# Performance work log

Measured on AMD Instinct MI355X. Metric: run time of the kernel, lower is better.

Reference implementation:

```python
import jax, jax.numpy as jnp
import numpy as np

TEMPERATURE = 0.07
BASE_TEMPERATURE = 0.07
EPS = 1e-10


def setup_inputs() -> dict:
    key = jax.random.key(0)
    k1, k2, k3 = jax.random.split(key, 3)
    bsz, n_views, d = 4096, 2, 256
    features = jax.random.normal(k1, (bsz, n_views, d), dtype=jnp.float32)
    # L2-normalize views as is standard for SupCon inputs (keeps logits sane)
    features = features / jnp.linalg.norm(features, axis=-1, keepdims=True)
    va_labels = jax.random.normal(k2, (bsz, 2), dtype=jnp.float32)
    batch_belong_diaID = jax.random.randint(k3, (bsz,), 0, 512, dtype=jnp.int64)
    return {
        "features": features,
        "va_labels": va_labels,
        "batch_belong_diaID": batch_belong_diaID,
        "thres_dict": 1,
    }


def reference(features, va_labels, batch_belong_diaID, thres_dict):
    bsz, n_views, d = features.shape
    dtype = features.dtype

    # --- vectorized mask construction (replaces O(bsz^2) python loops) ---
    eye = jnp.eye(bsz, dtype=bool)
    same_dia = batch_belong_diaID[:, None] == batch_belong_diaID[None, :]
    diff = va_labels[:, None, :] - va_labels[None, :, :]          # [bsz, bsz, 2]
    euclid = jnp.sqrt(jnp.sum(diff * diff, axis=-1))              # [bsz, bsz]
    close_va = euclid < thres_dict
    # final mask: diagonal | same dialogue | VA-close (off-diag terms; diag already 1)
    mask = (eye | same_dia | close_va).astype(dtype)
    mask = jax.lax.stop_gradient(mask)  # mask build is non-differentiable in torch too

    # --- contrastive loss (contrast_mode='one') ---
    # torch.cat(torch.unbind(features, 1), 0): view-major stacking
    contrast_feature = features.transpose(1, 0, 2).reshape(n_views * bsz, d)
    anchor_feature = features[:, 0]                               # anchor_count = 1

    logits = jnp.matmul(anchor_feature, contrast_feature.T) / TEMPERATURE  # [bsz, n_views*bsz]
    logits = logits - jax.lax.stop_gradient(jnp.max(logits, axis=1, keepdims=True))

    mask_t = jnp.tile(mask, (1, n_views))                          # [bsz, n_views*bsz]
    # logits_mask: zero out self-contrast (column i for anchor row i)
    idx = jnp.arange(bsz)
    logits_mask = jnp.ones((bsz, n_views * bsz), dtype=dtype).at[idx, idx].set(0.0)
    mask_t = mask_t * logits_mask

    exp_logits = jnp.exp(logits) * logits_mask
    log_prob = logits - jnp.log(jnp.sum(exp_logits, axis=1, keepdims=True) + EPS)

    mean_log_prob_pos = jnp.sum(mask_t * log_prob, axis=1) / (jnp.sum(mask_t, axis=1) + EPS)
    loss = jnp.mean(-mean_log_prob_pos)  # anchor_count=1 -> plain mean over bsz
    return loss
```

## Files before the change

kernel.cpp:

```cpp
#include <hip/hip_runtime.h>
#include <hip/hip_bf16.h>

#define BSZ   4096
#define NCON  8192
#define DFEAT 256
#define C2    20.60992914f
#define LN2   0.6931471806f

#define BJM 32
#define BI 128
#define NJT 8
#define JSTRIP_M (NJT * BJM)

typedef __attribute__((ext_vector_type(8))) short short8;
typedef __attribute__((ext_vector_type(4))) float f32x4;

__device__ __forceinline__ unsigned short f2bf(float f) {
    __hip_bfloat16 h = __float2bfloat16(f);
    return *reinterpret_cast<unsigned short*>(&h);
}

__device__ __forceinline__ void gload_lds16(const void* g, void* l) {
    __builtin_amdgcn_global_load_lds(
        (const __attribute__((address_space(1))) unsigned int*)g,
        (__attribute__((address_space(3))) unsigned int*)l,
        16, 0, 0);
}

__device__ __forceinline__ void gload_reg16(const void* p, short8& dst) {
    unsigned long long a = (unsigned long long)p;
    asm volatile("global_load_dwordx4 %0, %1, off"
                 : "=v"(dst) : "v"(a));
}


__global__ __launch_bounds__(256) void k_prep(const float* __restrict__ feat,
                                              unsigned short* __restrict__ con,
                                              float* __restrict__ acc) {
    int idx = blockIdx.x * 256 + threadIdx.x;
    int e = idx * 4;
    int j = e >> 8;
    int k = e & 255;
    int src = (j < BSZ) ? ((j * 2) * DFEAT + k)
                        : (((j - BSZ) * 2 + 1) * DFEAT + k);
    float4 f = *(const float4*)(feat + src);
    ushort4 o;
    o.x = f2bf(f.x); o.y = f2bf(f.y); o.z = f2bf(f.z); o.w = f2bf(f.w);
    *(ushort4*)(con + e) = o;
    if (idx < 3 * BSZ) acc[idx] = 0.0f;
}

__global__ __launch_bounds__(256, 2) void k_main(const __hip_bfloat16* __restrict__ conp,
                                                 const float* __restrict__ va,
                                                 const int* __restrict__ dia,
                                                 const int* __restrict__ thr_ptr,
                                                 float* __restrict__ Srow,
                                                 float* __restrict__ Arow,
                                                 float* __restrict__ Brow) {
    __shared__ short lX[2][2][BJM * DFEAT];
    __shared__ float s_vjx[JSTRIP_M], s_vjy[JSTRIP_M];
    __shared__ int   s_dj[JSTRIP_M];

    const int tid  = threadIdx.x;
    const int lane = tid & 63;
    const int wv   = tid >> 6;
    const int l15  = lane & 15;
    const int hi   = lane >> 4;
    const int jmbase = blockIdx.x * JSTRIP_M;
    const int ibase  = blockIdx.y * BI + wv * 32;
    const short* cs = (const short*)conp;

    auto stageX = [&](int buf, int jt) {
        #pragma unroll
        for (int v = 0; v < 2; ++v) {
            #pragma unroll
            for (int q = 0; q < 4; ++q) {
                int e   = q * 2048 + tid * 8;
                int col = e & 63;
                int row = (e >> 6) & 31;
                int k2  = e >> 11;
                int scol = col ^ ((row & 7) << 3);
                gload_lds16(cs + (size_t)(jmbase + jt * BJM + row + v * BSZ) * DFEAT
                               + k2 * 64 + scol,
                            &lX[buf][v][e]);
            }
        }
    };

    stageX(0, 0);

    const short* yrow0 = cs + (size_t)(ibase + l15) * DFEAT + hi * 8;
    short8 y[2][8];
    #pragma unroll
    for (int n = 0; n < 2; ++n)
        #pragma unroll
        for (int s = 0; s < 8; ++s)
            gload_reg16(yrow0 + (size_t)n * 16 * DFEAT + s * 32, y[n][s]);

    if (tid < JSTRIP_M) {
        int jm = jmbase + tid;
        s_vjx[tid] = va[2 * jm]; s_vjy[tid] = va[2 * jm + 1]; s_dj[tid] = dia[jm];
    }

    int raw = *thr_ptr;
    float t_ = (raw > 0 && raw < 100000) ? (float)raw : __int_as_float(raw);
    float thres2 = t_ * t_;

    float vix[2], viy[2]; int di[2], ig[2];
    #pragma unroll
    for (int n = 0; n < 2; ++n) {
        ig[n] = ibase + n * 16 + l15;
        vix[n] = va[2 * ig[n]]; viy[n] = va[2 * ig[n] + 1]; di[n] = dia[ig[n]];
    }

    float sp[2] = {0.f, 0.f};
    float ap[2] = {0.f, 0.f};
    float bp[2] = {0.f, 0.f};

    __syncthreads();
    asm volatile("s_waitcnt vmcnt(0)" ::: "memory");
    __builtin_amdgcn_sched_barrier(0);

    for (int jt = 0; jt < NJT; ++jt) {
        const int cur = jt & 1;
        if (jt < NJT - 1) stageX(cur ^ 1, jt + 1);

        f32x4 acc[2][2][2];
        #pragma unroll
        for (int v = 0; v < 2; ++v)
            #pragma unroll
            for (int m = 0; m < 2; ++m)
                #pragma unroll
                for (int n = 0; n < 2; ++n)
                    acc[v][m][n] = (f32x4){0.f, 0.f, 0.f, 0.f};

        __builtin_amdgcn_s_setprio(1);
        #pragma unroll
        for (int s = 0; s < 8; ++s) {
            const int base = (s >> 1) * 4096;
            const int colb = (s & 1) * 64 + hi * 16;
            short8 xf[2][2];
            #pragma unroll
            for (int v = 0; v < 2; ++v)
                #pragma unroll
                for (int m = 0; m < 2; ++m) {
                    int row = m * 16 + l15;
                    xf[v][m] = *(const short8*)((const char*)&lX[cur][v][0]
                                 + base + row * 128 + (colb ^ ((row & 7) << 4)));
                }
            #pragma unroll
            for (int v = 0; v < 2; ++v)
                #pragma unroll
                for (int m = 0; m < 2; ++m)
                    #pragma unroll
                    for (int n = 0; n < 2; ++n)
                        acc[v][m][n] = __builtin_amdgcn_mfma_f32_16x16x32_bf16(
                            xf[v][m], y[n][s], acc[v][m][n], 0, 0, 0);
        }
        __builtin_amdgcn_s_setprio(0);

        const int jt0 = jt * BJM;
        #pragma unroll
        for (int m = 0; m < 2; ++m)
            #pragma unroll
            for (int r = 0; r < 4; ++r) {
                const int jl  = jt0 + m * 16 + hi * 4 + r;
                const int jmg = jmbase + jl;
                float vjx = s_vjx[jl], vjy = s_vjy[jl];
                int dj = s_dj[jl];
                #pragma unroll
                for (int n = 0; n < 2; ++n) {
                    float l0 = __builtin_fmaf(acc[0][m][n][r], C2, -C2);
                    float l1 = __builtin_fmaf(acc[1][m][n][r], C2, -C2);
                    float dx = vix[n] - vjx, dy = viy[n] - vjy;
                    bool diag = (ig[n] == jmg);
                    bool mk = (di[n] == dj) | (dx * dx + dy * dy < thres2);
                    float e0 = diag ? 0.0f : exp2f(l0);
                    float e1 = exp2f(l1);
                    sp[n] += e0 + e1;
                    float mm = mk ? 1.0f : 0.0f;
                    ap[n] = __builtin_fmaf(mm, l0 + l1, ap[n]);
                    bp[n] += mm;
                }
            }
        __syncthreads();
    }

    #pragma unroll
    for (int n = 0; n < 2; ++n) {
        float s = sp[n], a = ap[n], b = bp[n];
        s += __shfl_xor(s, 16, 64);  a += __shfl_xor(a, 16, 64);  b += __shfl_xor(b, 16, 64);
        s += __shfl_xor(s, 32, 64);  a += __shfl_xor(a, 32, 64);  b += __shfl_xor(b, 32, 64);
        if (hi == 0) {
            atomicAdd(&Srow[ig[n]], s);
            atomicAdd(&Arow[ig[n]], a * LN2);
            atomicAdd(&Brow[ig[n]], b);
        }
    }
}

__global__ __launch_bounds__(256) void k_final(const float* __restrict__ S,
                                               const float* __restrict__ A,
                                               const float* __restrict__ B,
                                               float* __restrict__ out) {
    __shared__ float red[256];
    float sum = 0.f;
    for (int i = threadIdx.x; i < BSZ; i += 256) {
        float b = 2.0f * B[i] - 1.0f;
        float v = (A[i] - b * logf(S[i] + 1e-10f)) / (b + 1e-10f);
        sum += -v;
    }
    red[threadIdx.x] = sum;
    __syncthreads();
    for (int s = 128; s > 0; s >>= 1) {
        if (threadIdx.x < s) red[threadIdx.x] += red[threadIdx.x + s];
        __syncthreads();
    }
    if (threadIdx.x == 0) out[0] = red[0] / (float)BSZ;
}

extern "C" void kernel_launch(void* const* d_in, const int* in_sizes, int n_in,
                              void* d_out, int out_size, void* d_ws, size_t ws_size,
                              hipStream_t stream) {
    const float* feat = (const float*)d_in[0];
    const float* va   = (const float*)d_in[1];
    const int*   dia  = (const int*)d_in[2];
    const int*   thr  = (const int*)d_in[3];

    unsigned short* con = (unsigned short*)d_ws;
    float* acc = (float*)((char*)d_ws + (size_t)NCON * DFEAT * 2);
    float* out = (float*)d_out;

    k_prep<<<(NCON * DFEAT / 4 + 255) / 256, 256, 0, stream>>>(feat, con, acc);

    dim3 grid(BSZ / JSTRIP_M, BSZ / BI);
    k_main<<<grid, 256, 0, stream>>>((const __hip_bfloat16*)con, va, dia, thr,
                                     acc, acc + BSZ, acc + 2 * BSZ);

    k_final<<<1, 256, 0, stream>>>(acc, acc + BSZ, acc + 2 * BSZ, out);
}
```

Baseline: 47.01 us.

## Use 512-thread blocks with a four-stage LDS pipeline and per-view mask accounting

Doubles the anchor rows per block by going to 512 threads, so each staged contrast tile is reused by twice as many waves. Replaces double buffering with a 4-deep LDS ring that keeps three tiles in flight, using explicit vmcnt waits and a single s_barrier per tile in place of two __syncthreads. Also computes the positive mask and counts separately for the two views, so the self column is excluded only for view 0, and the final kernel uses the count directly instead of 2B-1. The larger LDS footprint and single-block occupancy can reduce latency hiding, and the hand-set vmcnt values must match the number of loads issued per thread.

```diff
diff --git a/kernel.cpp b/kernel.cpp
--- a/kernel.cpp
+++ b/kernel.cpp
@@ -8,7 +8,7 @@
 #define LN2   0.6931471806f
 
 #define BJM 32
-#define BI 128
+#define BI 256
 #define NJT 8
 #define JSTRIP_M (NJT * BJM)
 
@@ -50,14 +50,14 @@
     if (idx < 3 * BSZ) acc[idx] = 0.0f;
 }
 
-__global__ __launch_bounds__(256, 2) void k_main(const __hip_bfloat16* __restrict__ conp,
+__global__ __launch_bounds__(512, 1) void k_main(const __hip_bfloat16* __restrict__ conp,
                                                  const float* __restrict__ va,
                                                  const int* __restrict__ dia,
                                                  const int* __restrict__ thr_ptr,
                                                  float* __restrict__ Srow,
                                                  float* __restrict__ Arow,
                                                  float* __restrict__ Brow) {
-    __shared__ short lX[2][2][BJM * DFEAT];
+    __shared__ short lX[4][2][BJM * DFEAT];
     __shared__ float s_vjx[JSTRIP_M], s_vjy[JSTRIP_M];
     __shared__ int   s_dj[JSTRIP_M];
 
@@ -74,8 +74,8 @@
         #pragma unroll
         for (int v = 0; v < 2; ++v) {
             #pragma unroll
-            for (int q = 0; q < 4; ++q) {
-                int e   = q * 2048 + tid * 8;
+            for (int q = 0; q < 2; ++q) {
+                int e   = q * 4096 + tid * 8;
                 int col = e & 63;
                 int row = (e >> 6) & 31;
                 int k2  = e >> 11;
@@ -88,7 +88,7 @@
     };
 
     stageX(0, 0);
-
+    __builtin_amdgcn_sched_barrier(0);
     const short* yrow0 = cs + (size_t)(ibase + l15) * DFEAT + hi * 8;
     short8 y[2][8];
     #pragma unroll
@@ -96,6 +96,11 @@
         #pragma unroll
         for (int s = 0; s < 8; ++s)
             gload_reg16(yrow0 + (size_t)n * 16 * DFEAT + s * 32, y[n][s]);
+    __builtin_amdgcn_sched_barrier(0);
+    stageX(1, 1);
+    __builtin_amdgcn_sched_barrier(0);
+    stageX(2, 2);
+    __builtin_amdgcn_sched_barrier(0);
 
     if (tid < JSTRIP_M) {
         int jm = jmbase + tid;
@@ -117,14 +122,15 @@
     float ap[2] = {0.f, 0.f};
     float bp[2] = {0.f, 0.f};
 
-    __syncthreads();
-    asm volatile("s_waitcnt vmcnt(0)" ::: "memory");
-    __builtin_amdgcn_sched_barrier(0);
-
-    for (int jt = 0; jt < NJT; ++jt) {
-        const int cur = jt & 1;
-        if (jt < NJT - 1) stageX(cur ^ 1, jt + 1);
-
+    #pragma unroll
+    for (int t = 0; t < NJT; ++t) {
+        if (t <= 5)      asm volatile("s_waitcnt vmcnt(8)" ::: "memory");
+        else if (t == 6) asm volatile("s_waitcnt vmcnt(4)" ::: "memory");
+        else             asm volatile("s_waitcnt vmcnt(0)" ::: "memory");
+        __builtin_amdgcn_sched_barrier(0);
+        __builtin_amdgcn_s_barrier();
+
+        const int cur = t & 3;
         f32x4 acc[2][2][2];
         #pragma unroll
         for (int v = 0; v < 2; ++v)
@@ -134,7 +140,6 @@
                 for (int n = 0; n < 2; ++n)
                     acc[v][m][n] = (f32x4){0.f, 0.f, 0.f, 0.f};
 
-        __builtin_amdgcn_s_setprio(1);
         #pragma unroll
         for (int s = 0; s < 8; ++s) {
             const int base = (s >> 1) * 4096;
@@ -157,9 +162,8 @@
                         acc[v][m][n] = __builtin_amdgcn_mfma_f32_16x16x32_bf16(
                             xf[v][m], y[n][s], acc[v][m][n], 0, 0, 0);
         }
-        __builtin_amdgcn_s_setprio(0);
-
-        const int jt0 = jt * BJM;
+
+        const int jt0 = t * BJM;
         #pragma unroll
         for (int m = 0; m < 2; ++m)
             #pragma unroll
@@ -174,16 +178,19 @@
                     float l1 = __builtin_fmaf(acc[1][m][n][r], C2, -C2);
                     float dx = vix[n] - vjx, dy = viy[n] - vjy;
                     bool diag = (ig[n] == jmg);
-                    bool mk = (di[n] == dj) | (dx * dx + dy * dy < thres2);
+                    bool mk = diag | (di[n] == dj) | (dx * dx + dy * dy < thres2);
                     float e0 = diag ? 0.0f : exp2f(l0);
                     float e1 = exp2f(l1);
                     sp[n] += e0 + e1;
-                    float mm = mk ? 1.0f : 0.0f;
-                    ap[n] = __builtin_fmaf(mm, l0 + l1, ap[n]);
-                    bp[n] += mm;
+                    float m1f = mk ? 1.0f : 0.0f;
+                    float m0f = (mk & !diag) ? 1.0f : 0.0f;
+                    ap[n] = __builtin_fmaf(m0f, l0, ap[n]);
+                    ap[n] = __builtin_fmaf(m1f, l1, ap[n]);
+                    bp[n] += m0f + m1f;
                 }
             }
-        __syncthreads();
+
+        if (t < NJT - 3) stageX((t + 3) & 3, t + 3);
     }
 
     #pragma unroll
@@ -206,7 +213,7 @@
     __shared__ float red[256];
     float sum = 0.f;
     for (int i = threadIdx.x; i < BSZ; i += 256) {
-        float b = 2.0f * B[i] - 1.0f;
+        float b = B[i];
         float v = (A[i] - b * logf(S[i] + 1e-10f)) / (b + 1e-10f);
         sum += -v;
     }
@@ -234,7 +241,7 @@
     k_prep<<<(NCON * DFEAT / 4 + 255) / 256, 256, 0, stream>>>(feat, con, acc);
 
     dim3 grid(BSZ / JSTRIP_M, BSZ / BI);
-    k_main<<<grid, 256, 0, stream>>>((const __hip_bfloat16*)con, va, dia, thr,
+    k_main<<<grid, 512, 0, stream>>>((const __hip_bfloat16*)con, va, dia, thr,
                                      acc, acc + BSZ, acc + 2 * BSZ);
 
     k_final<<<1, 256, 0, stream>>>(acc, acc + BSZ, acc + 2 * BSZ, out);
```

Measured after the change: 68.93 us. +46.6%, slower.
